# Performance work log

Hardware: AMD Instinct MI355X
Metric: run time of the kernel (lower is better)

Reference implementation:

```python
import jax, jax.numpy as jnp
import numpy as np

RESIDUAL_SCALE = 0.002

def setup_inputs() -> dict:
    key = jax.random.key(0)
    x = jax.random.normal(key, (8, 128, 64, 64), dtype=jnp.float32)
    return {"x": x}

def reference(x):
    b, c, w, h = x.shape
    f = x.reshape(b, c, w * h)                      # [b, c, wh]
    # scores[b,i,j] = sum_c x[b,c,i] * x[b,c,j]  (hvi @ gui)
    scores = jnp.einsum('bci,bcj->bij', f, f)       # [b, wh, wh]
    # torch F.softmax(UiVi, 1): softmax over the first wh axis (axis=1)
    attn = jax.nn.softmax(scores, axis=1)
    # Ai = lui @ attn_map -> [b, c, wh]
    ai = jnp.einsum('bci,bij->bcj', f, attn)
    return x + RESIDUAL_SCALE * ai.reshape(b, c, w, h)
```

## Files before the change

### kernel.cpp

```cpp
#include <hip/hip_runtime.h>


typedef __bf16 bf16;
typedef bf16 bf16x2 __attribute__((ext_vector_type(2)));
typedef bf16 bf16x4 __attribute__((ext_vector_type(4)));
typedef bf16 bf16x8 __attribute__((ext_vector_type(8)));
typedef float f32x4 __attribute__((ext_vector_type(4)));
typedef float f32x16 __attribute__((ext_vector_type(16)));
typedef unsigned int u32;
typedef u32 u32x4 __attribute__((ext_vector_type(4)));

#define BATCH 8
#define CD 128
#define NN 4096
#define QBLK 128
#define KVB 64
#define NT (NN / KVB)
#define LOG2E 1.44269504f

#define KT_BY(row, colb) (((row) << 8) + ((colb) ^ (((row) & 7) << 4)))
#define VT_BY(row, colb) (((row) << 7) + ((colb) ^ (((row) & 7) << 4)))

__global__ __launch_bounds__(256) void transpose_to_bf16(const float* __restrict__ x,
                                                         bf16* __restrict__ ft) {
    const u32 g  = blockIdx.x * 256 + threadIdx.x;
    const u32 b  = g >> 16;
    const u32 r  = g & 65535;
    const u32 n_lo  = r & 15;
    const u32 c8_lo = (r >> 4) & 3;
    const u32 hi    = r >> 6;
    const u32 c8 = (hi & 3) * 4 + c8_lo;
    const u32 n  = (hi >> 2) * 16 + n_lo;
    const float* xb = x + (size_t)b * CD * NN;
    bf16x8 o;
#pragma unroll
    for (int e = 0; e < 8; e++)
        o[e] = (bf16)xb[(size_t)(c8 * 8 + e) * NN + n];
    *reinterpret_cast<bf16x8*>(ft + ((size_t)b * NN + n) * CD + c8 * 8) = o;
}

__global__ __launch_bounds__(512, 2) void attn_kernel(const float* __restrict__ x,
                                                      const bf16* __restrict__ ft,
                                                      float* __restrict__ out) {
    const int tid = threadIdx.x;
    const int w   = tid >> 6;
    const int wq  = w & 3;
    const int wk  = w >> 2;
    const int l   = tid & 63;
    const int l31 = l & 31;
    const int h   = l >> 5;

    const int batch = blockIdx.x & 7;
    const int q0    = (blockIdx.x >> 3) * QBLK;

    const bf16*  ftb  = ft  + (size_t)batch * NN * CD;
    const float* xb   = x   + (size_t)batch * CD * NN;
    float*       outb = out + (size_t)batch * CD * NN;

    __shared__ union {
        struct {
            bf16 kt[2][KVB * 128];
            bf16 vt[2][CD * 64];
        } s;
        float o[QBLK][133];
    } sm;
    __shared__ float s_mx[8][32], s_ls[8][32];

    bf16x8 qf[8];
    {
        const bf16* qp = ftb + (size_t)(q0 + wq * 32 + l31) * CD + h * 8;
#pragma unroll
        for (int kst = 0; kst < 8; kst++) {
            bf16x8 t = *reinterpret_cast<const bf16x8*>(qp + kst * 16);
#pragma unroll
            for (int e = 0; e < 8; e++) qf[kst][e] = (bf16)((float)t[e] * LOG2E);
        }
    }

    bf16x8 kreg[2];
    f32x4  vreg[4];
    auto stage_load = [&](int i0) {
#pragma unroll
        for (int j = 0; j < 2; j++) {
            const int slot = tid + j * 512;
            kreg[j] = *reinterpret_cast<const bf16x8*>(
                ftb + (size_t)(i0 + (slot >> 4)) * CD + (slot & 15) * 8);
        }
#pragma unroll
        for (int j = 0; j < 4; j++) {
            const int slot = tid + j * 512;
            vreg[j] = *reinterpret_cast<const f32x4*>(
                xb + (size_t)(slot >> 4) * NN + i0 + (slot & 15) * 4);
        }
    };
    auto stage_write = [&](int buf) {
        char* ktb = (char*)sm.s.kt[buf];
        char* vtb = (char*)sm.s.vt[buf];
#pragma unroll
        for (int j = 0; j < 2; j++) {
            const int slot = tid + j * 512;
            *reinterpret_cast<bf16x8*>(ktb + KT_BY(slot >> 4, (slot & 15) * 16)) = kreg[j];
        }
#pragma unroll
        for (int j = 0; j < 4; j++) {
            const int slot = tid + j * 512;
            bf16x4 t;
#pragma unroll
            for (int e = 0; e < 4; e++) t[e] = (bf16)vreg[j][e];
            *reinterpret_cast<bf16x4*>(vtb + VT_BY(slot >> 4, (slot & 15) * 8)) = t;
        }
    };

    f32x16 oacc[4];
#pragma unroll
    for (int ct = 0; ct < 4; ct++)
#pragma unroll
        for (int r = 0; r < 16; r++) oacc[ct][r] = 0.0f;
    float m_run = -1e30f;
    float l_par = 0.0f;

    stage_load(0);
    stage_write(0);
    __syncthreads();

    for (int it = 0; it < NT; ++it) {
        const int cur = it & 1;
        if (it + 1 < NT) stage_load((it + 1) * KVB);

        const char* ktb = (const char*)sm.s.kt[cur];
        const char* vtb = (const char*)sm.s.vt[cur];

        f32x16 sA, sB;
#pragma unroll
        for (int r = 0; r < 16; r++) { sA[r] = 0.0f; sB[r] = 0.0f; }
        __builtin_amdgcn_s_setprio(1);
#pragma unroll
        for (int kst = 0; kst < 8; kst += 2) {
            bf16x8 kf0 = *reinterpret_cast<const bf16x8*>(
                ktb + KT_BY(wk * 32 + l31, kst * 32 + h * 16));
            bf16x8 kf1 = *reinterpret_cast<const bf16x8*>(
                ktb + KT_BY(wk * 32 + l31, (kst + 1) * 32 + h * 16));
            sA = __builtin_amdgcn_mfma_f32_32x32x16_bf16(kf0, qf[kst], sA, 0, 0, 0);
            sB = __builtin_amdgcn_mfma_f32_32x32x16_bf16(kf1, qf[kst + 1], sB, 0, 0, 0);
        }
        __builtin_amdgcn_s_setprio(0);
        float s[16];
#pragma unroll
        for (int r = 0; r < 16; r++) s[r] = sA[r] + sB[r];

        float mp = s[0];
#pragma unroll
        for (int r = 1; r < 16; r++) mp = fmaxf(mp, s[r]);
        mp = fmaxf(mp, __shfl_xor(mp, 32));

        if (__any(mp > m_run + 11.5f)) {
            const float mn = fmaxf(m_run, mp);
            const float al = exp2f(m_run - mn);
            m_run = mn;
            l_par *= al;
#pragma unroll
            for (int ct = 0; ct < 4; ct++)
#pragma unroll
                for (int r = 0; r < 16; r++) oacc[ct][r] *= al;
        }

        float pe[16];
        float ps = 0.0f;
#pragma unroll
        for (int r = 0; r < 16; r++) { pe[r] = exp2f(s[r] - m_run); ps += pe[r]; }
        l_par += ps;

        u32 W[4][2], Xs[4][2];
#pragma unroll
        for (int gg = 0; gg < 4; gg++)
#pragma unroll
            for (int j = 0; j < 2; j++) {
                bf16x2 t = {(bf16)pe[4 * gg + 2 * j], (bf16)pe[4 * gg + 2 * j + 1]};
                W[gg][j] = __builtin_bit_cast(unsigned short, t[0]) |
                           ((u32)__builtin_bit_cast(unsigned short, t[1]) << 16);
                Xs[gg][j] = (u32)__shfl_xor((int)W[gg][j], 32);
            }
        u32x4 pw0 = {h ? Xs[1][0] : W[0][0], h ? Xs[1][1] : W[0][1],
                     h ? W[1][0] : Xs[0][0], h ? W[1][1] : Xs[0][1]};
        u32x4 pw1 = {h ? Xs[3][0] : W[2][0], h ? Xs[3][1] : W[2][1],
                     h ? W[3][0] : Xs[2][0], h ? W[3][1] : Xs[2][1]};
        bf16x8 pa0 = __builtin_bit_cast(bf16x8, pw0);
        bf16x8 pa1 = __builtin_bit_cast(bf16x8, pw1);

        __builtin_amdgcn_s_setprio(1);
#pragma unroll
        for (int ct = 0; ct < 4; ct++) {
            bf16x8 vf0 = *reinterpret_cast<const bf16x8*>(
                vtb + VT_BY(ct * 32 + l31, wk * 64 + h * 16));
            oacc[ct] = __builtin_amdgcn_mfma_f32_32x32x16_bf16(pa0, vf0, oacc[ct], 0, 0, 0);
            bf16x8 vf1 = *reinterpret_cast<const bf16x8*>(
                vtb + VT_BY(ct * 32 + l31, wk * 64 + 32 + h * 16));
            oacc[ct] = __builtin_amdgcn_mfma_f32_32x32x16_bf16(pa1, vf1, oacc[ct], 0, 0, 0);
        }
        __builtin_amdgcn_s_setprio(0);

        if (it + 1 < NT) stage_write(cur ^ 1);
        __syncthreads();
    }

    const float L = l_par + __shfl_xor(l_par, 32);
    if (l < 32) { s_mx[w][l31] = m_run; s_ls[w][l31] = L; }
    __syncthreads();
    const float m_o = s_mx[w ^ 4][l31];
    const float L_o = s_ls[w ^ 4][l31];
    const float m_p = fmaxf(m_run, m_o);
    const float eS  = exp2f(m_run - m_p);
    const float eO  = exp2f(m_o - m_p);
    const float fsc = eS / (L * eS + L_o * eO);

    if (wk == 0) {
#pragma unroll
        for (int ct = 0; ct < 4; ct++)
#pragma unroll
            for (int r = 0; r < 16; r++)
                sm.o[wq * 32 + l31][ct * 32 + (r & 3) + 8 * (r >> 2) + 4 * h] =
                    oacc[ct][r] * fsc;
    }
    __syncthreads();
    if (wk == 1) {
#pragma unroll
        for (int ct = 0; ct < 4; ct++)
#pragma unroll
            for (int r = 0; r < 16; r++)
                sm.o[wq * 32 + l31][ct * 32 + (r & 3) + 8 * (r >> 2) + 4 * h] +=
                    oacc[ct][r] * fsc;
    }
    __syncthreads();

#pragma unroll
    for (int k = 0; k < 8; k++) {
        const int slot = tid + k * 512;
        const int c  = slot >> 5;
        const int q4 = (slot & 31) * 4;
        f32x4 xv = *reinterpret_cast<const f32x4*>(xb + (size_t)c * NN + q0 + q4);
        f32x4 ov;
#pragma unroll
        for (int e = 0; e < 4; e++)
            ov[e] = xv[e] + 0.002f * sm.o[q4 + e][c];
        *reinterpret_cast<f32x4*>(outb + (size_t)c * NN + q0 + q4) = ov;
    }
}

extern "C" void kernel_launch(void* const* d_in, const int* in_sizes, int n_in,
                              void* d_out, int out_size, void* d_ws, size_t ws_size,
                              hipStream_t stream) {
    const float* x = (const float*)d_in[0];
    float* out = (float*)d_out;
    bf16* ft = (bf16*)d_ws;

    transpose_to_bf16<<<2048, 256, 0, stream>>>(x, ft);
    attn_kernel<<<256, 512, 0, stream>>>(x, ft, out);
}
```

Before: 178.4 us.

## Widen attention block to 16 waves with 128-key tiles and four-way key split

```diff
diff --git a/kernel.cpp b/kernel.cpp
--- a/kernel.cpp
+++ b/kernel.cpp
@@ -14,12 +14,12 @@
 #define CD 128
 #define NN 4096
 #define QBLK 128
-#define KVB 64
+#define KVB 128
 #define NT (NN / KVB)
 #define LOG2E 1.44269504f
 
 #define KT_BY(row, colb) (((row) << 8) + ((colb) ^ (((row) & 7) << 4)))
-#define VT_BY(row, colb) (((row) << 7) + ((colb) ^ (((row) & 7) << 4)))
+#define VT_BY(row, colb) (((row) << 8) + ((colb) ^ (((row) & 7) << 4)))
 
 __global__ __launch_bounds__(256) void transpose_to_bf16(const float* __restrict__ x,
                                                          bf16* __restrict__ ft) {
@@ -39,9 +39,9 @@
     *reinterpret_cast<bf16x8*>(ft + ((size_t)b * NN + n) * CD + c8 * 8) = o;
 }
 
-__global__ __launch_bounds__(512, 2) void attn_kernel(const float* __restrict__ x,
-                                                      const bf16* __restrict__ ft,
-                                                      float* __restrict__ out) {
+__global__ __launch_bounds__(1024, 4) void attn_kernel(const float* __restrict__ x,
+                                                       const bf16* __restrict__ ft,
+                                                       float* __restrict__ out) {
     const int tid = threadIdx.x;
     const int w   = tid >> 6;
     const int wq  = w & 3;
@@ -60,11 +60,11 @@
     __shared__ union {
         struct {
             bf16 kt[2][KVB * 128];
-            bf16 vt[2][CD * 64];
+            bf16 vt[2][CD * KVB];
         } s;
-        float o[QBLK][133];
+        float o[CD][132];
     } sm;
-    __shared__ float s_mx[8][32], s_ls[8][32];
+    __shared__ float s_mx[16][32], s_ls[16][32];
 
     bf16x8 qf[8];
     {
@@ -82,15 +82,15 @@
     auto stage_load = [&](int i0) {
 #pragma unroll
         for (int j = 0; j < 2; j++) {
-            const int slot = tid + j * 512;
+            const int slot = tid + j * 1024;
             kreg[j] = *reinterpret_cast<const bf16x8*>(
                 ftb + (size_t)(i0 + (slot >> 4)) * CD + (slot & 15) * 8);
         }
 #pragma unroll
         for (int j = 0; j < 4; j++) {
-            const int slot = tid + j * 512;
+            const int slot = tid + j * 1024;
             vreg[j] = *reinterpret_cast<const f32x4*>(
-                xb + (size_t)(slot >> 4) * NN + i0 + (slot & 15) * 4);
+                xb + (size_t)(slot >> 5) * NN + i0 + (slot & 31) * 4);
         }
     };
     auto stage_write = [&](int buf) {
@@ -98,16 +98,16 @@
         char* vtb = (char*)sm.s.vt[buf];
 #pragma unroll
         for (int j = 0; j < 2; j++) {
-            const int slot = tid + j * 512;
+            const int slot = tid + j * 1024;
             *reinterpret_cast<bf16x8*>(ktb + KT_BY(slot >> 4, (slot & 15) * 16)) = kreg[j];
         }
 #pragma unroll
         for (int j = 0; j < 4; j++) {
-            const int slot = tid + j * 512;
+            const int slot = tid + j * 1024;
             bf16x4 t;
 #pragma unroll
             for (int e = 0; e < 4; e++) t[e] = (bf16)vreg[j][e];
-            *reinterpret_cast<bf16x4*>(vtb + VT_BY(slot >> 4, (slot & 15) * 8)) = t;
+            *reinterpret_cast<bf16x4*>(vtb + VT_BY(slot >> 5, (slot & 31) * 8)) = t;
         }
     };
 
@@ -203,45 +203,46 @@
         __syncthreads();
     }
 
-    const float L = l_par + __shfl_xor(l_par, 32);
-    if (l < 32) { s_mx[w][l31] = m_run; s_ls[w][l31] = L; }
+    const float Lp = l_par + __shfl_xor(l_par, 32);
+    if (l < 32) { s_mx[w][l31] = m_run; s_ls[w][l31] = Lp; }
     __syncthreads();
-    const float m_o = s_mx[w ^ 4][l31];
-    const float L_o = s_ls[w ^ 4][l31];
-    const float m_p = fmaxf(m_run, m_o);
-    const float eS  = exp2f(m_run - m_p);
-    const float eO  = exp2f(m_o - m_p);
-    const float fsc = eS / (L * eS + L_o * eO);
-
-    if (wk == 0) {
-#pragma unroll
-        for (int ct = 0; ct < 4; ct++)
-#pragma unroll
-            for (int r = 0; r < 16; r++)
-                sm.o[wq * 32 + l31][ct * 32 + (r & 3) + 8 * (r >> 2) + 4 * h] =
-                    oacc[ct][r] * fsc;
-    }
-    __syncthreads();
-    if (wk == 1) {
-#pragma unroll
-        for (int ct = 0; ct < 4; ct++)
-#pragma unroll
-            for (int r = 0; r < 16; r++)
-                sm.o[wq * 32 + l31][ct * 32 + (r & 3) + 8 * (r >> 2) + 4 * h] +=
-                    oacc[ct][r] * fsc;
-    }
-    __syncthreads();
-
-#pragma unroll
-    for (int k = 0; k < 8; k++) {
-        const int slot = tid + k * 512;
+
+    float m_p = m_run;
+#pragma unroll
+    for (int j = 0; j < 4; j++) m_p = fmaxf(m_p, s_mx[wq + 4 * j][l31]);
+    float Lt = 0.0f;
+#pragma unroll
+    for (int j = 0; j < 4; j++)
+        Lt += s_ls[wq + 4 * j][l31] * exp2f(s_mx[wq + 4 * j][l31] - m_p);
+    const float fsc = exp2f(m_run - m_p) / Lt;
+
+#pragma unroll
+    for (int ph = 0; ph < 4; ph++) {
+        if (wk == ph) {
+#pragma unroll
+            for (int ct = 0; ct < 4; ct++)
+#pragma unroll
+                for (int r = 0; r < 16; r++) {
+                    const int c = ct * 32 + (r & 3) + 8 * (r >> 2) + 4 * h;
+                    const float v = oacc[ct][r] * fsc;
+                    if (ph == 0) sm.o[c][wq * 32 + l31] = v;
+                    else         sm.o[c][wq * 32 + l31] += v;
+                }
+        }
+        __syncthreads();
+    }
+
+#pragma unroll
+    for (int k = 0; k < 4; k++) {
+        const int slot = tid + k * 1024;
         const int c  = slot >> 5;
         const int q4 = (slot & 31) * 4;
         f32x4 xv = *reinterpret_cast<const f32x4*>(xb + (size_t)c * NN + q0 + q4);
+        f32x4 oo = *reinterpret_cast<const f32x4*>(&sm.o[c][q4]);
         f32x4 ov;
 #pragma unroll
         for (int e = 0; e < 4; e++)
-            ov[e] = xv[e] + 0.002f * sm.o[q4 + e][c];
+            ov[e] = xv[e] + 0.002f * oo[e];
         *reinterpret_cast<f32x4*>(outb + (size_t)c * NN + q0 + q4) = ov;
     }
 }
@@ -254,5 +255,5 @@
     bf16* ft = (bf16*)d_ws;
 
     transpose_to_bf16<<<2048, 256, 0, stream>>>(x, ft);
-    attn_kernel<<<256, 512, 0, stream>>>(x, ft, out);
+    attn_kernel<<<256, 1024, 0, stream>>>(x, ft, out);
 }
```

Result: slower. 511.5 us (+186.7%).

## Pre-convert V to bf16, use permlane32 swap, transpose output staging

Applied to the files above, without the earlier changes.

```diff
diff --git a/kernel.cpp b/kernel.cpp
--- a/kernel.cpp
+++ b/kernel.cpp
@@ -39,8 +39,20 @@
     *reinterpret_cast<bf16x8*>(ft + ((size_t)b * NN + n) * CD + c8 * 8) = o;
 }
 
+__global__ __launch_bounds__(256) void to_bf16(const float* __restrict__ x,
+                                               bf16* __restrict__ xh) {
+    const int i = blockIdx.x * 256 + threadIdx.x;
+    f32x4 v = reinterpret_cast<const f32x4*>(x)[i];
+    bf16x4 o;
+#pragma unroll
+    for (int e = 0; e < 4; e++) o[e] = (bf16)v[e];
+    reinterpret_cast<bf16x4*>(xh)[i] = o;
+}
+
+template <bool XH>
 __global__ __launch_bounds__(512, 2) void attn_kernel(const float* __restrict__ x,
                                                       const bf16* __restrict__ ft,
+                                                      const bf16* __restrict__ xh,
                                                       float* __restrict__ out) {
     const int tid = threadIdx.x;
     const int w   = tid >> 6;
@@ -54,15 +66,16 @@
     const int q0    = (blockIdx.x >> 3) * QBLK;
 
     const bf16*  ftb  = ft  + (size_t)batch * NN * CD;
+    const bf16*  xhb  = XH ? xh + (size_t)batch * CD * NN : nullptr;
     const float* xb   = x   + (size_t)batch * CD * NN;
     float*       outb = out + (size_t)batch * CD * NN;
 
     __shared__ union {
         struct {
             bf16 kt[2][KVB * 128];
-            bf16 vt[2][CD * 64];
+            bf16 vt[2][CD * KVB];
         } s;
-        float o[QBLK][133];
+        float o[CD][132];
     } sm;
     __shared__ float s_mx[8][32], s_ls[8][32];
 
@@ -78,7 +91,8 @@
     }
 
     bf16x8 kreg[2];
-    f32x4  vreg[4];
+    bf16x8 vregh[2];
+    f32x4  vregf[4];
     auto stage_load = [&](int i0) {
 #pragma unroll
         for (int j = 0; j < 2; j++) {
@@ -86,11 +100,20 @@
             kreg[j] = *reinterpret_cast<const bf16x8*>(
                 ftb + (size_t)(i0 + (slot >> 4)) * CD + (slot & 15) * 8);
         }
-#pragma unroll
-        for (int j = 0; j < 4; j++) {
-            const int slot = tid + j * 512;
-            vreg[j] = *reinterpret_cast<const f32x4*>(
-                xb + (size_t)(slot >> 4) * NN + i0 + (slot & 15) * 4);
+        if constexpr (XH) {
+#pragma unroll
+            for (int j = 0; j < 2; j++) {
+                const int slot = tid + j * 512;
+                vregh[j] = *reinterpret_cast<const bf16x8*>(
+                    xhb + (size_t)(slot >> 3) * NN + i0 + (slot & 7) * 8);
+            }
+        } else {
+#pragma unroll
+            for (int j = 0; j < 4; j++) {
+                const int slot = tid + j * 512;
+                vregf[j] = *reinterpret_cast<const f32x4*>(
+                    xb + (size_t)(slot >> 4) * NN + i0 + (slot & 15) * 4);
+            }
         }
     };
     auto stage_write = [&](int buf) {
@@ -101,13 +124,21 @@
             const int slot = tid + j * 512;
             *reinterpret_cast<bf16x8*>(ktb + KT_BY(slot >> 4, (slot & 15) * 16)) = kreg[j];
         }
-#pragma unroll
-        for (int j = 0; j < 4; j++) {
-            const int slot = tid + j * 512;
-            bf16x4 t;
-#pragma unroll
-            for (int e = 0; e < 4; e++) t[e] = (bf16)vreg[j][e];
-            *reinterpret_cast<bf16x4*>(vtb + VT_BY(slot >> 4, (slot & 15) * 8)) = t;
+        if constexpr (XH) {
+#pragma unroll
+            for (int j = 0; j < 2; j++) {
+                const int slot = tid + j * 512;
+                *reinterpret_cast<bf16x8*>(vtb + VT_BY(slot >> 3, (slot & 7) * 16)) = vregh[j];
+            }
+        } else {
+#pragma unroll
+            for (int j = 0; j < 4; j++) {
+                const int slot = tid + j * 512;
+                bf16x4 t;
+#pragma unroll
+                for (int e = 0; e < 4; e++) t[e] = (bf16)vregf[j][e];
+                *reinterpret_cast<bf16x4*>(vtb + VT_BY(slot >> 4, (slot & 15) * 8)) = t;
+            }
         }
     };
 
@@ -170,7 +201,7 @@
         for (int r = 0; r < 16; r++) { pe[r] = exp2f(s[r] - m_run); ps += pe[r]; }
         l_par += ps;
 
-        u32 W[4][2], Xs[4][2];
+        u32 W[4][2];
 #pragma unroll
         for (int gg = 0; gg < 4; gg++)
 #pragma unroll
@@ -178,12 +209,13 @@
                 bf16x2 t = {(bf16)pe[4 * gg + 2 * j], (bf16)pe[4 * gg + 2 * j + 1]};
                 W[gg][j] = __builtin_bit_cast(unsigned short, t[0]) |
                            ((u32)__builtin_bit_cast(unsigned short, t[1]) << 16);
-                Xs[gg][j] = (u32)__shfl_xor((int)W[gg][j], 32);
-            }
-        u32x4 pw0 = {h ? Xs[1][0] : W[0][0], h ? Xs[1][1] : W[0][1],
-                     h ? W[1][0] : Xs[0][0], h ? W[1][1] : Xs[0][1]};
-        u32x4 pw1 = {h ? Xs[3][0] : W[2][0], h ? Xs[3][1] : W[2][1],
-                     h ? W[3][0] : Xs[2][0], h ? W[3][1] : Xs[2][1]};
+            }
+        asm volatile("v_permlane32_swap_b32 %0, %1" : "+v"(W[0][0]), "+v"(W[1][0]));
+        asm volatile("v_permlane32_swap_b32 %0, %1" : "+v"(W[0][1]), "+v"(W[1][1]));
+        asm volatile("v_permlane32_swap_b32 %0, %1" : "+v"(W[2][0]), "+v"(W[3][0]));
+        asm volatile("v_permlane32_swap_b32 %0, %1" : "+v"(W[2][1]), "+v"(W[3][1]));
+        u32x4 pw0 = {W[0][0], W[0][1], W[1][0], W[1][1]};
+        u32x4 pw1 = {W[2][0], W[2][1], W[3][0], W[3][1]};
         bf16x8 pa0 = __builtin_bit_cast(bf16x8, pw0);
         bf16x8 pa1 = __builtin_bit_cast(bf16x8, pw1);
 
@@ -203,32 +235,35 @@
         __syncthreads();
     }
 
-    const float L = l_par + __shfl_xor(l_par, 32);
-    if (l < 32) { s_mx[w][l31] = m_run; s_ls[w][l31] = L; }
+    const float Lp = l_par + __shfl_xor(l_par, 32);
+    if (l < 32) { s_mx[w][l31] = m_run; s_ls[w][l31] = Lp; }
     __syncthreads();
+
     const float m_o = s_mx[w ^ 4][l31];
     const float L_o = s_ls[w ^ 4][l31];
     const float m_p = fmaxf(m_run, m_o);
     const float eS  = exp2f(m_run - m_p);
     const float eO  = exp2f(m_o - m_p);
-    const float fsc = eS / (L * eS + L_o * eO);
+    const float fsc = 0.002f * eS / (Lp * eS + L_o * eO);
 
     if (wk == 0) {
 #pragma unroll
         for (int ct = 0; ct < 4; ct++)
 #pragma unroll
-            for (int r = 0; r < 16; r++)
-                sm.o[wq * 32 + l31][ct * 32 + (r & 3) + 8 * (r >> 2) + 4 * h] =
-                    oacc[ct][r] * fsc;
+            for (int r = 0; r < 16; r++) {
+                const int c = ct * 32 + (r & 3) + 8 * (r >> 2) + 4 * h;
+                sm.o[c][wq * 32 + l31] = oacc[ct][r] * fsc;
+            }
     }
     __syncthreads();
     if (wk == 1) {
 #pragma unroll
         for (int ct = 0; ct < 4; ct++)
 #pragma unroll
-            for (int r = 0; r < 16; r++)
-                sm.o[wq * 32 + l31][ct * 32 + (r & 3) + 8 * (r >> 2) + 4 * h] +=
-                    oacc[ct][r] * fsc;
+            for (int r = 0; r < 16; r++) {
+                const int c = ct * 32 + (r & 3) + 8 * (r >> 2) + 4 * h;
+                sm.o[c][wq * 32 + l31] += oacc[ct][r] * fsc;
+            }
     }
     __syncthreads();
 
@@ -238,10 +273,11 @@
         const int c  = slot >> 5;
         const int q4 = (slot & 31) * 4;
         f32x4 xv = *reinterpret_cast<const f32x4*>(xb + (size_t)c * NN + q0 + q4);
+        f32x4 oo = *reinterpret_cast<const f32x4*>(&sm.o[c][q4]);
         f32x4 ov;
 #pragma unroll
         for (int e = 0; e < 4; e++)
-            ov[e] = xv[e] + 0.002f * sm.o[q4 + e][c];
+            ov[e] = xv[e] + oo[e];
         *reinterpret_cast<f32x4*>(outb + (size_t)c * NN + q0 + q4) = ov;
     }
 }
@@ -252,7 +288,16 @@
     const float* x = (const float*)d_in[0];
     float* out = (float*)d_out;
     bf16* ft = (bf16*)d_ws;
+    bf16* xh = ft + (size_t)BATCH * NN * CD;
+
+    const bool use_xh = ws_size >= ((size_t)32u << 20) ? true
+                       : ws_size >= ((size_t)16u << 20);
 
     transpose_to_bf16<<<2048, 256, 0, stream>>>(x, ft);
-    attn_kernel<<<256, 512, 0, stream>>>(x, ft, out);
+    if (use_xh) {
+        to_bf16<<<4096, 256, 0, stream>>>(x, xh);
+        attn_kernel<true><<<256, 512, 0, stream>>>(x, ft, xh, out);
+    } else {
+        attn_kernel<false><<<256, 512, 0, stream>>>(x, ft, nullptr, out);
+    }
 }
```

Measured after the change: 176.1 us. Within noise of the previous version (-1.3%).
